# Kernel tuning notes

Hardware: AMD Instinct MI355X
Metric: run time of the kernel (lower is better)

The kernel has to match this reference:

```python
import jax, jax.numpy as jnp
import numpy as np

B, S, D, H, DC, HC = 2, 2048, 1024, 16, 64, 16  # batch, seq, hidden, heads, coord_dim, head_coord_dim
HD = D // H  # head_dim


def setup_inputs() -> dict:
    key = jax.random.key(0)
    ks = jax.random.split(key, 12)
    s = lambda fan_in: 1.0 / np.sqrt(fan_in)
    return {
        "hidden_states": jax.random.normal(ks[0], (B, S, D), jnp.float32),
        "coordinates": jax.random.normal(ks[1], (B, S, DC), jnp.float32),
        # weights stored [in, out] (used as x @ W + b, equivalent to torch Linear)
        "Wv": jax.random.uniform(ks[2], (D, D), jnp.float32, -s(D), s(D)),
        "bv": jax.random.uniform(ks[3], (D,), jnp.float32, -s(D), s(D)),
        "Wc": jax.random.uniform(ks[4], (DC, H * HC), jnp.float32, -s(DC), s(DC)),
        "bc": jax.random.uniform(ks[5], (H * HC,), jnp.float32, -s(DC), s(DC)),
        "Wn": jax.random.uniform(ks[6], (DC, DC), jnp.float32, -s(DC), s(DC)),
        "bn": jax.random.uniform(ks[7], (DC,), jnp.float32, -s(DC), s(DC)),
        "Wo": jax.random.uniform(ks[8], (D, D), jnp.float32, -s(D), s(D)),
        "bo": jax.random.uniform(ks[9], (D,), jnp.float32, -s(D), s(D)),
        "gamma": jax.random.normal(ks[10], (1, H, 1, 1), jnp.float32),
    }


def reference(hidden_states, coordinates, Wv, bv, Wc, bc, Wn, bn, Wo, bo, gamma):
    b, s, _ = hidden_states.shape
    # value: [B,H,S,HD]
    value = (hidden_states @ Wv + bv).reshape(b, s, H, HD).transpose(0, 2, 1, 3)
    # coord heads: [B,H,S,HC]
    z = (coordinates @ Wc + bc).reshape(b, s, H, HC).transpose(0, 2, 1, 3)
    z_sq = jnp.sum(z * z, axis=-1, keepdims=True)  # [B,H,S,1]
    sq_dist = z_sq + jnp.swapaxes(z_sq, -1, -2) - 2.0 * jnp.einsum("bhsc,bhtc->bhst", z, z)
    sq_dist = jnp.maximum(sq_dist, 0.0)
    g = jax.nn.softplus(gamma)  # [1,H,1,1]
    attn = jax.nn.softmax(-g * sq_dist, axis=-1)  # [B,H,S,S]
    out = jnp.einsum("bhst,bhtd->bhsd", attn, value)
    out = out.transpose(0, 2, 1, 3).reshape(b, s, D)
    updated_hidden = out @ Wo + bo
    updated_coords = coordinates @ Wn + bn
    return (updated_hidden, updated_coords)
```

## Files before the change

### kernel.cpp

```cpp
#include <hip/hip_runtime.h>
#include <hip/hip_bf16.h>

typedef short bf16x8 __attribute__((ext_vector_type(8)));
typedef float f32x4 __attribute__((ext_vector_type(4)));
typedef float f32x16 __attribute__((ext_vector_type(16)));
typedef unsigned short u16;
typedef unsigned int u32;

__device__ __forceinline__ u16 f2b(float f) {
  __hip_bfloat16 h = __float2bfloat16(f);
  return *reinterpret_cast<u16*>(&h);
}

#define MFMA16(a, b, c) __builtin_amdgcn_mfma_f32_16x16x32_bf16((a), (b), (c), 0, 0, 0)
#define MFMA32(a, b, c) __builtin_amdgcn_mfma_f32_32x32x16_bf16((a), (b), (c), 0, 0, 0)


__global__ void k_cvt(const float* __restrict__ in, u16* __restrict__ out, int n) {
  int i = (blockIdx.x * 256 + threadIdx.x) * 4;
  if (i >= n) return;
  float4 v = *reinterpret_cast<const float4*>(in + i);
  ushort4 o;
  o.x = f2b(v.x); o.y = f2b(v.y); o.z = f2b(v.z); o.w = f2b(v.w);
  *reinterpret_cast<ushort4*>(out + i) = o;
}

__global__ void k_wT(const float* __restrict__ W, u16* __restrict__ WT) {
  __shared__ float t[64][65];
  int tid = threadIdx.x;
  int r0 = (blockIdx.x & 15) << 6;
  int c0 = (blockIdx.x >> 4) << 6;
#pragma unroll
  for (int rep = 0; rep < 4; ++rep) {
    int e = tid + rep * 256;
    int r = e >> 4, c4 = (e & 15) << 2;
    float4 v = *reinterpret_cast<const float4*>(W + (size_t)(r0 + r) * 1024 + c0 + c4);
    t[r][c4] = v.x; t[r][c4 + 1] = v.y; t[r][c4 + 2] = v.z; t[r][c4 + 3] = v.w;
  }
  __syncthreads();
#pragma unroll
  for (int rep = 0; rep < 4; ++rep) {
    int e = tid + rep * 256;
    int c = e >> 4, r4 = (e & 15) << 2;
    ushort4 o;
    o.x = f2b(t[r4][c]); o.y = f2b(t[r4 + 1][c]);
    o.z = f2b(t[r4 + 2][c]); o.w = f2b(t[r4 + 3][c]);
    *reinterpret_cast<ushort4*>(WT + (size_t)(c0 + c) * 1024 + r0 + r4) = o;
  }
}

__global__ void k_z(const float* __restrict__ C, const float* __restrict__ Wc,
                    const float* __restrict__ bc, const float* __restrict__ gamma,
                    u16* __restrict__ Z, u16* __restrict__ Zg, u32* __restrict__ zghl) {
  int gid = blockIdx.x * 256 + threadIdx.x;
  int bs = gid >> 4, h = gid & 15;
  float gm = gamma[h];
  float g = (gm > 15.f) ? gm : log1pf(__expf(gm));
  float g2 = g * 1.4426950408889634f;
  float tg2 = 2.f * g2;
  const float* crow = C + (size_t)bs * 64;
  float acc[16];
#pragma unroll
  for (int c = 0; c < 16; ++c) acc[c] = bc[h * 16 + c];
  for (int k = 0; k < 64; ++k) {
    float cv = crow[k];
    const float* wr = Wc + (size_t)k * 256 + h * 16;
#pragma unroll
    for (int c = 0; c < 16; ++c) acc[c] = fmaf(cv, wr[c], acc[c]);
  }
  float sq = 0.f;
  u16 tz[16], tg[16];
#pragma unroll
  for (int c = 0; c < 16; ++c) {
    sq += acc[c] * acc[c];
    tz[c] = f2b(acc[c]);
    tg[c] = f2b(tg2 * acc[c]);
  }
  float x = -g2 * sq;
  u32 xu = __float_as_uint(x);
  float xh = __uint_as_float(xu & 0xFFFF0000u);
  u32 packed = (xu >> 16) | ((u32)f2b(x - xh) << 16);
  int b = bs >> 11, s = bs & 2047;
  int bh = (b << 4) + h;
  size_t ro = (((size_t)bh << 11) + s) * 16;
  *reinterpret_cast<uint4*>(Z + ro) = *reinterpret_cast<uint4*>(tz);
  *reinterpret_cast<uint4*>(Z + ro + 8) = *reinterpret_cast<uint4*>(tz + 8);
  *reinterpret_cast<uint4*>(Zg + ro) = *reinterpret_cast<uint4*>(tg);
  *reinterpret_cast<uint4*>(Zg + ro + 8) = *reinterpret_cast<uint4*>(tg + 8);
  zghl[((size_t)bh << 11) + s] = packed;
}

__global__ void k_coords(const float* __restrict__ C, const float* __restrict__ Wn,
                         const float* __restrict__ bn, float* __restrict__ out) {
  int gid = blockIdx.x * 256 + threadIdx.x;
  int bs = gid >> 6, c = gid & 63;
  const float* crow = C + (size_t)bs * 64;
  float acc = bn[c];
#pragma unroll 8
  for (int k = 0; k < 64; ++k) acc = fmaf(crow[k], Wn[k * 64 + c], acc);
  out[gid] = acc;
}

template <int OUTM>
__global__ __launch_bounds__(512, 4) void k_gemm(const u16* __restrict__ A,
                                                 const u16* __restrict__ BT,
                                                 const float* __restrict__ bias,
                                                 void* __restrict__ Cout,
                                                 int M, int N, int K) {
  __shared__ u16 As[128 * 64];
  __shared__ u16 Bs[64 * 64];
  int nbn = N >> 6;
  int bm = blockIdx.x / nbn, bn = blockIdx.x % nbn;
  int tid = threadIdx.x, lane = tid & 63, w = tid >> 6;
  int wm = w >> 1, wn = w & 1;
  int l15 = lane & 15, lg = lane >> 4;
  int lr = lane >> 3;
  int swc = (lane & 7) ^ lr;

  f32x4 acc[2][2];
#pragma unroll
  for (int mi = 0; mi < 2; ++mi)
#pragma unroll
    for (int ni = 0; ni < 2; ++ni) acc[mi][ni] = (f32x4){0.f, 0.f, 0.f, 0.f};

  const u16* Abase = A + (size_t)(bm * 128 + w * 8 + lr) * K + swc * 8;
  const u16* Bbase = BT + (size_t)(bn * 64 + w * 8 + lr) * K + swc * 8;
  int rsw = l15 & 7;

  for (int kk0 = 0; kk0 < K; kk0 += 64) {
    __syncthreads();
#pragma unroll
    for (int i = 0; i < 2; ++i)
      __builtin_amdgcn_global_load_lds(
          (const __attribute__((address_space(1))) u32*)(Abase + (size_t)(i * 64) * K + kk0),
          (__attribute__((address_space(3))) u32*)&As[(i * 64 + w * 8) * 64], 16, 0, 0);
    __builtin_amdgcn_global_load_lds(
        (const __attribute__((address_space(1))) u32*)(Bbase + kk0),
        (__attribute__((address_space(3))) u32*)&Bs[(w * 8) * 64], 16, 0, 0);
    __syncthreads();
#pragma unroll
    for (int kk = 0; kk < 2; ++kk) {
      int ch = (kk * 4 + lg) ^ rsw;
      bf16x8 af[2], bfr[2];
#pragma unroll
      for (int mi = 0; mi < 2; ++mi)
        af[mi] = *reinterpret_cast<const bf16x8*>(&As[(wm * 32 + mi * 16 + l15) * 64 + ch * 8]);
#pragma unroll
      for (int ni = 0; ni < 2; ++ni)
        bfr[ni] = *reinterpret_cast<const bf16x8*>(&Bs[(wn * 32 + ni * 16 + l15) * 64 + ch * 8]);
#pragma unroll
      for (int mi = 0; mi < 2; ++mi)
#pragma unroll
        for (int ni = 0; ni < 2; ++ni)
          acc[mi][ni] = MFMA16(af[mi], bfr[ni], acc[mi][ni]);
    }
  }
#pragma unroll
  for (int mi = 0; mi < 2; ++mi) {
#pragma unroll
    for (int ni = 0; ni < 2; ++ni) {
      int col = bn * 64 + wn * 32 + ni * 16 + l15;
      float bv = bias[col];
      if (OUTM == 0) {
#pragma unroll
        for (int j = 0; j < 4; ++j) {
          int row = bm * 128 + wm * 32 + mi * 16 + lg * 4 + j;
          reinterpret_cast<float*>(Cout)[(size_t)row * N + col] = acc[mi][ni][j] + bv;
        }
      } else {
        int row0 = bm * 128 + wm * 32 + mi * 16 + lg * 4;
        int b = row0 >> 11, tg = (row0 >> 4) & 127;
        int hi_ = lg >> 1, jb = (lg & 1) << 2;
        int h = col >> 6, hd = col & 63, dh = hd >> 5, lv = hd & 31;
        size_t addr = ((((size_t)(b * 16 + h) * 128 + tg) * 2 + dh) << 9) +
                      ((hi_ * 32 + lv) << 3) + jb;
        ushort4 o;
        o.x = f2b(acc[mi][ni][0] + bv); o.y = f2b(acc[mi][ni][1] + bv);
        o.z = f2b(acc[mi][ni][2] + bv); o.w = f2b(acc[mi][ni][3] + bv);
        *reinterpret_cast<ushort4*>(reinterpret_cast<u16*>(Cout) + addr) = o;
      }
    }
  }
}

__global__ __launch_bounds__(256, 2) void k_attn(const u16* __restrict__ Z,
                                                 const u16* __restrict__ Zg,
                                                 const u32* __restrict__ zghl,
                                                 const u16* __restrict__ VF,
                                                 u16* __restrict__ O) {
  __shared__ __align__(16) char smem[33792];
  float* psqf = reinterpret_cast<float*>(smem + 32768);

  int tid = threadIdx.x, lane = tid & 63, w = tid >> 6;
  int l31 = lane & 31, hi = lane >> 5;
  int hi4 = hi << 2, hi8 = hi << 3;
  int th = w & 1, qh = w >> 1, th32 = th << 5;
  int bh = blockIdx.x >> 4, qt = blockIdx.x & 15;
  int q0 = qt << 7;
  int h = bh & 15, bb = bh >> 4;

  const u16* Zb = Z + ((size_t)bh << 11) * 16;
  const u16* Zgb = Zg + ((size_t)bh << 11) * 16;
  const u32* ghl = zghl + ((size_t)bh << 11);
  const u16* VFb = VF + ((size_t)bh << 17);

  int qx0 = (qh << 6) + l31;
  int qx1 = qx0 + 32;

  bf16x8 zq2_0 = *reinterpret_cast<const bf16x8*>(Zgb + (size_t)(q0 + qx0) * 16 + hi8);
  bf16x8 zq2_1 = *reinterpret_cast<const bf16x8*>(Zgb + (size_t)(q0 + qx1) * 16 + hi8);

  u32 gq0 = ghl[q0 + qx0], gq1 = ghl[q0 + qx1];
  uint4 ab0 = {0x3F803F80u, gq0, 0u, 0u};
  uint4 ab1 = {0x3F803F80u, gq1, 0u, 0u};
  if (hi) { ab0.x = 0u; ab0.y = 0u; ab1.x = 0u; ab1.y = 0u; }
  bf16x8 aug_b0 = *reinterpret_cast<bf16x8*>(&ab0);
  bf16x8 aug_b1 = *reinterpret_cast<bf16x8*>(&ab1);

  uint4 aqu = {0u, 0x3F803F80u, 0u, 0u};
  if (hi) aqu.y = 0u;
  bf16x8 aug_q = *reinterpret_cast<bf16x8*>(&aqu);
  f32x16 qpart0 = MFMA32(aug_q, aug_b0, (f32x16){});
  f32x16 qpart1 = MFMA32(aug_q, aug_b1, (f32x16){});

  const u16* zap = Zb + (size_t)(th32 + l31) * 16 + hi8;
  const u32* xtp = ghl + th32 + l31;
  const u16* vwp = VFb + ((size_t)th << 11) + ((size_t)lane << 3);

  f32x16 oacc00 = {}, oacc01 = {}, oacc10 = {}, oacc11 = {};
  f32x4 ps0 = {}, ps1 = {};

  int swz = (l31 ^ (l31 >> 2)) & 3;
  char* pbase = smem + (w << 12) + l31 * 64;

  bf16x8 zA_c = *reinterpret_cast<const bf16x8*>(zap);
  u32 zhl_c = xtp[0];

#pragma unroll 2
  for (int tt = 0; tt < 32; ++tt) {
    const int t0 = tt << 6;
    const u16* vtb = vwp + (tt << 12);
    bf16x8 vb00 = *reinterpret_cast<const bf16x8*>(vtb);
    bf16x8 vb01 = *reinterpret_cast<const bf16x8*>(vtb + 512);
    bf16x8 vb10 = *reinterpret_cast<const bf16x8*>(vtb + 1024);
    bf16x8 vb11 = *reinterpret_cast<const bf16x8*>(vtb + 1536);
    bf16x8 zA_n = zA_c;
    u32 zhl_n = zhl_c;
    if (tt < 31) {
      zA_n = *reinterpret_cast<const bf16x8*>(zap + (size_t)(t0 + 64) * 16);
      zhl_n = xtp[t0 + 64];
    }

    uint4 aau = {hi ? 0u : zhl_c, 0u, 0u, 0u};
    bf16x8 aug_a = *reinterpret_cast<bf16x8*>(&aau);

    f32x16 sc0 = MFMA32(aug_a, aug_b0, qpart0);
    sc0 = MFMA32(zA_c, zq2_0, sc0);
    f32x16 sc1 = MFMA32(aug_a, aug_b1, qpart1);
    sc1 = MFMA32(zA_c, zq2_1, sc1);

    char* pb = pbase + ((tt & 1) << 14);
#pragma unroll
    for (int g = 0; g < 4; ++g) {
      int cb = ((g ^ swz) << 4) + (hi << 3);
      {
        float e0 = fminf(sc0[g * 4 + 0], 0.f), e1 = fminf(sc0[g * 4 + 1], 0.f);
        float e2 = fminf(sc0[g * 4 + 2], 0.f), e3 = fminf(sc0[g * 4 + 3], 0.f);
        float p0 = __builtin_amdgcn_exp2f(e0), p1 = __builtin_amdgcn_exp2f(e1);
        float p2 = __builtin_amdgcn_exp2f(e2), p3 = __builtin_amdgcn_exp2f(e3);
        ps0[0] += p0; ps0[1] += p1; ps0[2] += p2; ps0[3] += p3;
        u32 pk0, pk1;
        asm("v_cvt_pk_bf16_f32 %0, %1, %2" : "=v"(pk0) : "v"(p0), "v"(p1));
        asm("v_cvt_pk_bf16_f32 %0, %1, %2" : "=v"(pk1) : "v"(p2), "v"(p3));
        uint2 pkv = {pk0, pk1};
        *reinterpret_cast<uint2*>(pb + cb) = pkv;
      }
      {
        float e0 = fminf(sc1[g * 4 + 0], 0.f), e1 = fminf(sc1[g * 4 + 1], 0.f);
        float e2 = fminf(sc1[g * 4 + 2], 0.f), e3 = fminf(sc1[g * 4 + 3], 0.f);
        float p0 = __builtin_amdgcn_exp2f(e0), p1 = __builtin_amdgcn_exp2f(e1);
        float p2 = __builtin_amdgcn_exp2f(e2), p3 = __builtin_amdgcn_exp2f(e3);
        ps1[0] += p0; ps1[1] += p1; ps1[2] += p2; ps1[3] += p3;
        u32 pk0, pk1;
        asm("v_cvt_pk_bf16_f32 %0, %1, %2" : "=v"(pk0) : "v"(p0), "v"(p1));
        asm("v_cvt_pk_bf16_f32 %0, %1, %2" : "=v"(pk1) : "v"(p2), "v"(p3));
        uint2 pkv = {pk0, pk1};
        *reinterpret_cast<uint2*>(pb + 2048 + cb) = pkv;
      }
    }

    int c0b = (((0 * 2 + hi) ^ swz) << 4);
    int c1b = (((1 * 2 + hi) ^ swz) << 4);
    bf16x8 pa00 = *reinterpret_cast<const bf16x8*>(pb + c0b);
    bf16x8 pa01 = *reinterpret_cast<const bf16x8*>(pb + c1b);
    bf16x8 pa10 = *reinterpret_cast<const bf16x8*>(pb + 2048 + c0b);
    bf16x8 pa11 = *reinterpret_cast<const bf16x8*>(pb + 2048 + c1b);

    oacc00 = MFMA32(pa00, vb00, oacc00);
    oacc01 = MFMA32(pa00, vb01, oacc01);
    oacc10 = MFMA32(pa10, vb00, oacc10);
    oacc11 = MFMA32(pa10, vb01, oacc11);
    oacc00 = MFMA32(pa01, vb10, oacc00);
    oacc01 = MFMA32(pa01, vb11, oacc01);
    oacc10 = MFMA32(pa11, vb10, oacc10);
    oacc11 = MFMA32(pa11, vb11, oacc11);

    zA_c = zA_n; zhl_c = zhl_n;
  }

  float psum0 = (ps0[0] + ps0[1]) + (ps0[2] + ps0[3]);
  float psum1 = (ps1[0] + ps1[1]) + (ps1[2] + ps1[3]);
  psum0 += __shfl_xor(psum0, 32, 64);
  psum1 += __shfl_xor(psum1, 32, 64);

  __syncthreads();
  if (th == 1) {
    char* dst = smem + ((w >> 1) << 14) + lane * 16;
#pragma unroll
    for (int r = 0; r < 4; ++r) {
      *reinterpret_cast<f32x4*>(dst + (0 + r) * 1024) =
          (f32x4){oacc00[r * 4], oacc00[r * 4 + 1], oacc00[r * 4 + 2], oacc00[r * 4 + 3]};
      *reinterpret_cast<f32x4*>(dst + (4 + r) * 1024) =
          (f32x4){oacc01[r * 4], oacc01[r * 4 + 1], oacc01[r * 4 + 2], oacc01[r * 4 + 3]};
      *reinterpret_cast<f32x4*>(dst + (8 + r) * 1024) =
          (f32x4){oacc10[r * 4], oacc10[r * 4 + 1], oacc10[r * 4 + 2], oacc10[r * 4 + 3]};
      *reinterpret_cast<f32x4*>(dst + (12 + r) * 1024) =
          (f32x4){oacc11[r * 4], oacc11[r * 4 + 1], oacc11[r * 4 + 2], oacc11[r * 4 + 3]};
    }
  }
  if (lane < 32) {
    psqf[(w * 2 + 0) * 32 + l31] = psum0;
    psqf[(w * 2 + 1) * 32 + l31] = psum1;
  }
  __syncthreads();
  if (th == 0) {
    const char* src = smem + ((w >> 1) << 14) + lane * 16;
#pragma unroll
    for (int r = 0; r < 4; ++r) {
      f32x4 v0 = *reinterpret_cast<const f32x4*>(src + (0 + r) * 1024);
      f32x4 v1 = *reinterpret_cast<const f32x4*>(src + (4 + r) * 1024);
      f32x4 v2 = *reinterpret_cast<const f32x4*>(src + (8 + r) * 1024);
      f32x4 v3 = *reinterpret_cast<const f32x4*>(src + (12 + r) * 1024);
#pragma unroll
      for (int j = 0; j < 4; ++j) {
        oacc00[r * 4 + j] += v0[j];
        oacc01[r * 4 + j] += v1[j];
        oacc10[r * 4 + j] += v2[j];
        oacc11[r * 4 + j] += v3[j];
      }
    }
#pragma unroll
    for (int qbk = 0; qbk < 2; ++qbk) {
#pragma unroll
      for (int g = 0; g < 4; ++g) {
        f32x4 a = *reinterpret_cast<const f32x4*>(&psqf[(w * 2 + qbk) * 32 + (g << 3) + hi4]);
        f32x4 b2 = *reinterpret_cast<const f32x4*>(&psqf[((w + 1) * 2 + qbk) * 32 + (g << 3) + hi4]);
#pragma unroll
        for (int j = 0; j < 4; ++j) {
          float inv = __builtin_amdgcn_rcpf(a[j] + b2[j]);
          int qrow = (g << 3) + hi4 + j;
          int srow = q0 + (qh << 6) + (qbk << 5) + qrow;
          u16* orow = O + ((size_t)(bb * 2048 + srow) << 10) + h * 64 + l31;
          float v0 = (qbk ? oacc10[g * 4 + j] : oacc00[g * 4 + j]);
          float v1 = (qbk ? oacc11[g * 4 + j] : oacc01[g * 4 + j]);
          orow[0] = f2b(v0 * inv);
          orow[32] = f2b(v1 * inv);
        }
      }
    }
  }
}

extern "C" void kernel_launch(void* const* d_in, const int* in_sizes, int n_in,
                              void* d_out, int out_size, void* d_ws, size_t ws_size,
                              hipStream_t stream) {
  const float* hs     = (const float*)d_in[0];
  const float* coords = (const float*)d_in[1];
  const float* Wv     = (const float*)d_in[2];
  const float* bv     = (const float*)d_in[3];
  const float* Wc     = (const float*)d_in[4];
  const float* bc     = (const float*)d_in[5];
  const float* Wn     = (const float*)d_in[6];
  const float* bn     = (const float*)d_in[7];
  const float* Wo     = (const float*)d_in[8];
  const float* bo     = (const float*)d_in[9];
  const float* gamma  = (const float*)d_in[10];
  float* out_h = (float*)d_out;
  float* out_c = out_h + 4194304;

  char* ws = (char*)d_ws;
  u16*   HSb  = (u16*)(ws + 0);
  u16*   O    = (u16*)(ws + 0);
  u16*   WvT  = (u16*)(ws + 8388608);
  u16*   WoT  = (u16*)(ws + 10485760);
  u16*   Zw   = (u16*)(ws + 12582912);
  u16*   Zgw  = (u16*)(ws + 14680064);
  u32*   zghl = (u32*)(ws + 16777216);
  u16*   VFw  = (u16*)(ws + 17039360);

  k_cvt<<<4096, 256, 0, stream>>>(hs, HSb, 4194304);
  k_wT<<<256, 256, 0, stream>>>(Wv, WvT);
  k_wT<<<256, 256, 0, stream>>>(Wo, WoT);
  k_z<<<256, 256, 0, stream>>>(coords, Wc, bc, gamma, Zw, Zgw, zghl);
  k_gemm<1><<<512, 512, 0, stream>>>(HSb, WvT, bv, VFw, 4096, 1024, 1024);
  k_attn<<<512, 256, 0, stream>>>(Zw, Zgw, zghl, VFw, O);
  k_gemm<0><<<512, 512, 0, stream>>>(O, WoT, bo, out_h, 4096, 1024, 1024);
  k_coords<<<1024, 256, 0, stream>>>(coords, Wn, bn, out_c);
}
```

Before: 114.7 us.

## Double-buffer GEMM LDS tiles and raise wave priority around attention MFMAs

The bf16 GEMM kernel now keeps two LDS buffers for the A and B tiles and prefetches the next K-slice with global_load_lds while the current slice is computed. It uses an explicit vmcnt wait plus s_barrier in place of the two __syncthreads per iteration, so global loads overlap the MFMA work. The attention kernel also raises wave priority with s_setprio during the PV MFMA block. In exchange, LDS per block doubles to 48 KB, which may reduce occupancy under launch_bounds(512,4).

```diff
diff --git a/kernel.cpp b/kernel.cpp
--- a/kernel.cpp
+++ b/kernel.cpp
@@ -107,8 +107,8 @@
                                                  const float* __restrict__ bias,
                                                  void* __restrict__ Cout,
                                                  int M, int N, int K) {
-  __shared__ u16 As[128 * 64];
-  __shared__ u16 Bs[64 * 64];
+  __shared__ u16 As[2][128 * 64];
+  __shared__ u16 Bs[2][64 * 64];
   int nbn = N >> 6;
   int bm = blockIdx.x / nbn, bn = blockIdx.x % nbn;
   int tid = threadIdx.x, lane = tid & 63, w = tid >> 6;
@@ -127,34 +127,52 @@
   const u16* Bbase = BT + (size_t)(bn * 64 + w * 8 + lr) * K + swc * 8;
   int rsw = l15 & 7;
 
-  for (int kk0 = 0; kk0 < K; kk0 += 64) {
-    __syncthreads();
-#pragma unroll
-    for (int i = 0; i < 2; ++i)
-      __builtin_amdgcn_global_load_lds(
-          (const __attribute__((address_space(1))) u32*)(Abase + (size_t)(i * 64) * K + kk0),
-          (__attribute__((address_space(3))) u32*)&As[(i * 64 + w * 8) * 64], 16, 0, 0);
-    __builtin_amdgcn_global_load_lds(
-        (const __attribute__((address_space(1))) u32*)(Bbase + kk0),
-        (__attribute__((address_space(3))) u32*)&Bs[(w * 8) * 64], 16, 0, 0);
-    __syncthreads();
+#define GSTAGE(BUF, KK)                                                             \
+  do {                                                                              \
+    __builtin_amdgcn_global_load_lds(                                               \
+        (const __attribute__((address_space(1))) u32*)(Abase + (KK)),               \
+        (__attribute__((address_space(3))) u32*)&As[(BUF)][(w * 8) * 64], 16, 0, 0);\
+    __builtin_amdgcn_global_load_lds(                                               \
+        (const __attribute__((address_space(1))) u32*)(Abase + (size_t)64 * K + (KK)),\
+        (__attribute__((address_space(3))) u32*)&As[(BUF)][(64 + w * 8) * 64], 16, 0, 0);\
+    __builtin_amdgcn_global_load_lds(                                               \
+        (const __attribute__((address_space(1))) u32*)(Bbase + (KK)),               \
+        (__attribute__((address_space(3))) u32*)&Bs[(BUF)][(w * 8) * 64], 16, 0, 0);\
+  } while (0)
+
+  const int nk = K >> 6;
+  GSTAGE(0, 0);
+  for (int it = 0; it < nk; ++it) {
+    int cur = it & 1;
+    if (it + 1 < nk) {
+      GSTAGE(cur ^ 1, (it + 1) * 64);
+      asm volatile("s_waitcnt vmcnt(3)" ::: "memory");
+    } else {
+      asm volatile("s_waitcnt vmcnt(0)" ::: "memory");
+    }
+    __builtin_amdgcn_sched_barrier(0);
+    __builtin_amdgcn_s_barrier();
 #pragma unroll
     for (int kk = 0; kk < 2; ++kk) {
       int ch = (kk * 4 + lg) ^ rsw;
       bf16x8 af[2], bfr[2];
 #pragma unroll
       for (int mi = 0; mi < 2; ++mi)
-        af[mi] = *reinterpret_cast<const bf16x8*>(&As[(wm * 32 + mi * 16 + l15) * 64 + ch * 8]);
+        af[mi] = *reinterpret_cast<const bf16x8*>(&As[cur][(wm * 32 + mi * 16 + l15) * 64 + ch * 8]);
 #pragma unroll
       for (int ni = 0; ni < 2; ++ni)
-        bfr[ni] = *reinterpret_cast<const bf16x8*>(&Bs[(wn * 32 + ni * 16 + l15) * 64 + ch * 8]);
+        bfr[ni] = *reinterpret_cast<const bf16x8*>(&Bs[cur][(wn * 32 + ni * 16 + l15) * 64 + ch * 8]);
 #pragma unroll
       for (int mi = 0; mi < 2; ++mi)
 #pragma unroll
         for (int ni = 0; ni < 2; ++ni)
           acc[mi][ni] = MFMA16(af[mi], bfr[ni], acc[mi][ni]);
     }
-  }
+    __builtin_amdgcn_sched_barrier(0);
+    __builtin_amdgcn_s_barrier();
+  }
+#undef GSTAGE
+
 #pragma unroll
   for (int mi = 0; mi < 2; ++mi) {
 #pragma unroll
@@ -296,6 +314,7 @@
     bf16x8 pa10 = *reinterpret_cast<const bf16x8*>(pb + 2048 + c0b);
     bf16x8 pa11 = *reinterpret_cast<const bf16x8*>(pb + 2048 + c1b);
 
+    __builtin_amdgcn_s_setprio(1);
     oacc00 = MFMA32(pa00, vb00, oacc00);
     oacc01 = MFMA32(pa00, vb01, oacc01);
     oacc10 = MFMA32(pa10, vb00, oacc10);
@@ -304,6 +323,7 @@
     oacc01 = MFMA32(pa01, vb11, oacc01);
     oacc10 = MFMA32(pa11, vb10, oacc10);
     oacc11 = MFMA32(pa11, vb11, oacc11);
+    __builtin_amdgcn_s_setprio(0);
 
     zA_c = zA_n; zhl_c = zhl_n;
   }
```

Measured after the change: 110.3 us. 3.8% less time.
